# Kernel optimization log

Hardware: AMD Instinct MI355X
Metric: run time of the kernel (lower is better)

Reference implementation:

```python
import jax, jax.numpy as jnp
import numpy as np

B, T, C = 4, 2048, 768
H, D = 12, 64          # num heads, head size
MLP = 3072
EPS = 1e-6
SCALE = C ** (-0.5)    # NOTE: source scales by n_embd**-0.5, not head_size**-0.5


def setup_inputs() -> dict:
    key = jax.random.key(0)
    ks = jax.random.split(key, 12)
    s = 0.02
    return {
        "x":     jax.random.normal(ks[0], (B, T, C), jnp.float32),
        "Wq":    jax.random.normal(ks[1], (H, C, D), jnp.float32) * s,
        "Wk":    jax.random.normal(ks[2], (H, C, D), jnp.float32) * s,
        "Wv":    jax.random.normal(ks[3], (H, C, D), jnp.float32) * s,
        "Wo":    jax.random.normal(ks[4], (H * D, C), jnp.float32) * s,
        "bo":    jnp.zeros((C,), jnp.float32),
        "ln1_g": jnp.ones((C,), jnp.float32),
        "ln1_b": jnp.zeros((C,), jnp.float32),
        "ln2_g": jnp.ones((C,), jnp.float32),
        "ln2_b": jnp.zeros((C,), jnp.float32),
        "W1":    jax.random.normal(ks[5], (C, MLP), jnp.float32) * s,
        "b1":    jnp.zeros((MLP,), jnp.float32),
        "W2":    jax.random.normal(ks[6], (MLP, C), jnp.float32) * s,
        "b2":    jnp.zeros((C,), jnp.float32),
    }


def _ln(x, g, b):
    mu = jnp.mean(x, axis=-1, keepdims=True)
    var = jnp.var(x, axis=-1, keepdims=True)
    return (x - mu) * jax.lax.rsqrt(var + EPS) * g + b


def reference(x, Wq, Wk, Wv, Wo, bo, ln1_g, ln1_b, ln2_g, ln2_b, W1, b1, W2, b2):
    xn = _ln(x, ln1_g, ln1_b)
    # batched per-head projections: [B,T,C] x [H,C,D] -> [B,H,T,D]
    q = jnp.einsum("btc,hcd->bhtd", xn, Wq)
    k = jnp.einsum("btc,hcd->bhtd", xn, Wk)
    v = jnp.einsum("btc,hcd->bhtd", xn, Wv)
    wei = jnp.einsum("bhtd,bhsd->bhts", q, k) * SCALE  # [B,H,T,T]
    wei = jax.nn.softmax(wei, axis=-1)
    attn = jnp.einsum("bhts,bhsd->bhtd", wei, v)
    # concat heads along feature dim (head order preserved)
    attn = attn.transpose(0, 2, 1, 3).reshape(B, T, H * D)
    sa = attn @ Wo + bo
    x2 = sa + x                      # residual 1 (dropout = identity in eval)
    y = _ln(x2, ln2_g, ln2_b)
    y = jax.nn.gelu(y @ W1 + b1, approximate=False) @ W2 + b2
    return x2 + y                    # residual 2
```

## Files before the change

### kernel.cpp

```cpp
#include <hip/hip_runtime.h>
#include <hip/hip_bf16.h>
#include <cstdint>
#include <cmath>

#define B_ 4
#define T_ 2048
#define C_ 768
#define H_ 12
#define D_ 64
#define MLP_ 3072
#define BT_ (B_*T_)

typedef __hip_bfloat16 hbf;
typedef __bf16 bf16_t;
typedef bf16_t bf16x8 __attribute__((ext_vector_type(8)));
typedef bf16_t bf16x4 __attribute__((ext_vector_type(4)));
typedef float f32x4 __attribute__((ext_vector_type(4)));

static __device__ __forceinline__ void load_lds16(const void* g, void* l) {
    __builtin_amdgcn_global_load_lds(
        (const __attribute__((address_space(1))) unsigned int*)g,
        (__attribute__((address_space(3))) unsigned int*)l, 16, 0, 0);
}

__global__ __launch_bounds__(256) void transpose_pack(
    const float* __restrict__ src, hbf* __restrict__ dst, int R, int S)
{
    __shared__ float tl[64 * 65];
    src += (size_t)blockIdx.z * R * S;
    dst += (size_t)blockIdx.z * R * S;
    const int r0 = blockIdx.y * 64, s0 = blockIdx.x * 64;
    const int c = threadIdx.x & 63, q = threadIdx.x >> 6;
#pragma unroll
    for (int j = 0; j < 16; ++j) {
        int r = q + j * 4;
        tl[r * 65 + c] = src[(size_t)(r0 + r) * S + s0 + c];
    }
    __syncthreads();
#pragma unroll
    for (int j = 0; j < 16; ++j) {
        int s = q + j * 4;
        dst[(size_t)(s0 + s) * R + r0 + c] = __float2bfloat16(tl[c * 65 + s]);
    }
}

__global__ __launch_bounds__(256) void ln_kernel(
    const float* __restrict__ x, const float* __restrict__ g,
    const float* __restrict__ bb, hbf* __restrict__ out)
{
    __shared__ float red[8];
    const int row = blockIdx.x;
    const float* xr = x + (size_t)row * C_;
    const int t = threadIdx.x;
    float v0 = xr[t], v1 = xr[t + 256], v2 = xr[t + 512];
    float s = v0 + v1 + v2;
    float s2 = v0 * v0 + v1 * v1 + v2 * v2;
#pragma unroll
    for (int m = 1; m < 64; m <<= 1) {
        s  += __shfl_xor(s,  m, 64);
        s2 += __shfl_xor(s2, m, 64);
    }
    if ((t & 63) == 0) { red[t >> 6] = s; red[4 + (t >> 6)] = s2; }
    __syncthreads();
    float S  = red[0] + red[1] + red[2] + red[3];
    float S2 = red[4] + red[5] + red[6] + red[7];
    float mu  = S * (1.0f / C_);
    float var = S2 * (1.0f / C_) - mu * mu;
    float inv = rsqrtf(var + 1e-6f);
    hbf* orow = out + (size_t)row * C_;
    orow[t]       = __float2bfloat16((v0 - mu) * inv * g[t]       + bb[t]);
    orow[t + 256] = __float2bfloat16((v1 - mu) * inv * g[t + 256] + bb[t + 256]);
    orow[t + 512] = __float2bfloat16((v2 - mu) * inv * g[t + 512] + bb[t + 512]);
}

template<int EPI>
__global__ __launch_bounds__(256, 2) void gemm_kernel(
    const hbf* __restrict__ A, const hbf* __restrict__ Bt,
    float* __restrict__ outF, hbf* __restrict__ outH,
    const float* __restrict__ bias, const float* __restrict__ resid,
    int M, int N, int K,
    hbf* __restrict__ qb, hbf* __restrict__ kb,
    float scale, int gx)
{
    __shared__ hbf sA0[128 * 64], sA1[128 * 64];
    __shared__ hbf sB0[128 * 64], sB1[128 * 64];
    const int tid = threadIdx.x;
    const int lane = tid & 63;
    const int wid = tid >> 6;
    const int wm = wid >> 1, wn = wid & 1;
    const int lr = lane & 15, hg = lane >> 4;
    const int bid = blockIdx.x, nwg = gridDim.x;
    const int wg = (bid & 7) * (nwg >> 3) + (bid >> 3);
    const int bx = wg % gx, by = wg / gx;
    const int row0 = by * 128;
    const int col0 = bx * 128;

    f32x4 acc[4][4] = {};

    int offG[4];
    const int Kb = K * 2;
#pragma unroll
    for (int i = 0; i < 4; ++i) {
        int c = tid + i * 256;
        offG[i] = (c >> 3) * Kb + (((c & 7) ^ ((c >> 3) & 7)) << 4);
    }
    const char* gA = (const char*)(A + (size_t)row0 * K);
    const char* gB = (const char*)(Bt + (size_t)col0 * K);

    auto stage = [&](int kt, hbf* sAd, hbf* sBd) {
        const int kb2 = kt * 128;
#pragma unroll
        for (int i = 0; i < 4; ++i) {
            load_lds16(gA + (size_t)(offG[i] + kb2), (char*)sAd + i * 4096 + wid * 1024);
            load_lds16(gB + (size_t)(offG[i] + kb2), (char*)sBd + i * 4096 + wid * 1024);
        }
    };
    auto compute = [&](const hbf* sAc, const hbf* sBc) {
#pragma unroll
        for (int kf = 0; kf < 2; ++kf) {
            const int sl = ((kf * 4 + hg) ^ (lr & 7)) << 4;
            bf16x8 af[4], bfr[4];
#pragma unroll
            for (int m = 0; m < 4; ++m)
                af[m] = *(const bf16x8*)((const char*)sAc + (wm * 64 + m * 16 + lr) * 128 + sl);
#pragma unroll
            for (int n = 0; n < 4; ++n)
                bfr[n] = *(const bf16x8*)((const char*)sBc + (wn * 64 + n * 16 + lr) * 128 + sl);
#pragma unroll
            for (int m = 0; m < 4; ++m)
#pragma unroll
                for (int n = 0; n < 4; ++n)
                    acc[m][n] = __builtin_amdgcn_mfma_f32_16x16x32_bf16(af[m], bfr[n], acc[m][n], 0, 0, 0);
        }
    };

    const int NK = K >> 6;
    stage(0, sA0, sB0);
    __syncthreads();
    for (int kt = 0; kt < NK; kt += 2) {
        stage(kt + 1, sA1, sB1);
        compute(sA0, sB0);
        __syncthreads();
        if (kt + 2 < NK) stage(kt + 2, sA0, sB0);
        compute(sA1, sB1);
        __syncthreads();
    }

#pragma unroll
    for (int m = 0; m < 4; ++m) {
#pragma unroll
        for (int n = 0; n < 4; ++n) {
#pragma unroll
            for (int j = 0; j < 4; ++j) {
                int row = row0 + wm * 64 + m * 16 + hg * 4 + j;
                int col = col0 + wn * 64 + n * 16 + lr;
                float v = acc[m][n][j];
                if constexpr (EPI == 0) {
                    outH[(size_t)row * N + col] = __float2bfloat16(v);
                } else if constexpr (EPI == 1) {
                    outF[(size_t)row * N + col] = v + bias[col] + resid[(size_t)row * N + col];
                } else if constexpr (EPI == 2) {
                    float tt = v + bias[col];
                    float ge = 0.5f * tt * (1.0f + erff(tt * 0.70710678118654752f));
                    outH[(size_t)row * N + col] = __float2bfloat16(ge);
                } else {
                    int typ = col / C_;
                    int rr = col - typ * C_;
                    int h = rr >> 6, d = rr & 63;
                    int b = row >> 11, t = row & (T_ - 1);
                    size_t bh = (size_t)b * H_ + h;
                    if (typ == 0) qb[(bh * T_ + t) * D_ + d] = __float2bfloat16(v * scale);
                    else          kb[(bh * T_ + t) * D_ + d] = __float2bfloat16(v);
                }
            }
        }
    }
}

__global__ __launch_bounds__(256, 3) void attn_kernel(
    const hbf* __restrict__ qg, const hbf* __restrict__ kg,
    const hbf* __restrict__ vg, hbf* __restrict__ outA)
{
    __shared__ hbf sK0[64 * 64], sK1[64 * 64];
    __shared__ hbf sV0[64 * 64], sV1[64 * 64];
    __shared__ hbf sP[4 * 32 * 64];
    const int tid = threadIdx.x, lane = tid & 63, wid = tid >> 6;
    const int lr = lane & 15, hg = lane >> 4;
    const int wg = (blockIdx.x & 7) * 96 + (blockIdx.x >> 3);
    const int bh = wg >> 4;
    const int b = bh / H_, h = bh - b * H_;
    const int wr0 = (wg & 15) * 128 + wid * 32;
    const hbf* qbh = qg + (size_t)bh * T_ * D_;
    const hbf* kbh = kg + (size_t)bh * T_ * D_;
    const hbf* vbh = vg + (size_t)h * 64 * BT_ + (size_t)b * T_;

    bf16x8 a_q[2][2];
#pragma unroll
    for (int m = 0; m < 2; ++m)
#pragma unroll
        for (int kf = 0; kf < 2; ++kf)
            a_q[m][kf] = *(const bf16x8*)(qbh + (size_t)(wr0 + m * 16 + lr) * D_ + kf * 32 + hg * 8);

    f32x4 o[2][4] = {};
    float mreg[2] = {-3e38f, -3e38f};
    float lrun[2] = {0.0f, 0.0f};

    int offK[2], offV[2];
#pragma unroll
    for (int i = 0; i < 2; ++i) {
        int c = tid + i * 256;
        int sw = ((c & 7) ^ ((c >> 3) & 7)) << 4;
        offK[i] = (c >> 3) * 128 + sw;
        offV[i] = (c >> 3) * (BT_ * 2) + sw;
    }
    hbf* sPw = sP + wid * (32 * 64);
    const int sl0 = ((0 * 4 + hg) ^ (lr & 7)) << 4;
    const int sl1 = ((1 * 4 + hg) ^ (lr & 7)) << 4;
    const int bcast = hg * 20;

    auto stage = [&](int itn, hbf* sKd, hbf* sVd) {
        const char* kp = (const char*)kbh + (size_t)itn * 8192;
        const char* vp = (const char*)vbh + (size_t)itn * 128;
#pragma unroll
        for (int i = 0; i < 2; ++i) {
            load_lds16(kp + offK[i], (char*)sKd + i * 4096 + wid * 1024);
            load_lds16(vp + offV[i], (char*)sVd + i * 4096 + wid * 1024);
        }
    };

    auto tile = [&](const hbf* sKc, const hbf* sVc) {
        f32x4 st[4][2] = {};
        __builtin_amdgcn_s_setprio(1);
#pragma unroll
        for (int kf = 0; kf < 2; ++kf) {
            const int sl = kf ? sl1 : sl0;
#pragma unroll
            for (int n = 0; n < 4; ++n) {
                bf16x8 ak = *(const bf16x8*)((const char*)sKc + (n * 16 + lr) * 128 + sl);
                st[n][0] = __builtin_amdgcn_mfma_f32_16x16x32_bf16(ak, a_q[0][kf], st[n][0], 0, 0, 0);
                st[n][1] = __builtin_amdgcn_mfma_f32_16x16x32_bf16(ak, a_q[1][kf], st[n][1], 0, 0, 0);
            }
        }
        __builtin_amdgcn_s_setprio(0);

#pragma unroll
        for (int m = 0; m < 2; ++m) {
            float t = st[0][m][0];
#pragma unroll
            for (int n = 0; n < 4; ++n)
#pragma unroll
                for (int j = 0; j < 4; ++j)
                    if (n + j > 0) t = fmaxf(t, st[n][m][j]);
            t = fmaxf(t, __shfl_xor(t, 16, 64));
            t = fmaxf(t, __shfl_xor(t, 32, 64));
            if (__any(t - mreg[m] > 8.0f)) {
                float nm = fmaxf(mreg[m], t);
                float fac = __expf(mreg[m] - nm);
                mreg[m] = nm;
                lrun[m] *= fac;
                float fb[4];
#pragma unroll
                for (int j = 0; j < 4; ++j)
                    fb[j] = __shfl(fac, bcast + j, 64);
#pragma unroll
                for (int nd = 0; nd < 4; ++nd)
#pragma unroll
                    for (int j = 0; j < 4; ++j)
                        o[m][nd][j] *= fb[j];
            }
            float ps = 0.0f;
            const int r = m * 16 + lr;
#pragma unroll
            for (int n = 0; n < 4; ++n) {
                float p0 = __expf(st[n][m][0] - mreg[m]);
                float p1 = __expf(st[n][m][1] - mreg[m]);
                float p2 = __expf(st[n][m][2] - mreg[m]);
                float p3 = __expf(st[n][m][3] - mreg[m]);
                ps += (p0 + p1) + (p2 + p3);
                bf16x4 w;
                w[0] = (bf16_t)p0; w[1] = (bf16_t)p1; w[2] = (bf16_t)p2; w[3] = (bf16_t)p3;
                *(bf16x4*)((char*)sPw + r * 128 +
                           (((n * 2 + (hg >> 1)) ^ (r & 7)) << 4) + ((hg & 1) * 8)) = w;
            }
            ps += __shfl_xor(ps, 16, 64);
            ps += __shfl_xor(ps, 32, 64);
            lrun[m] += ps;
        }

        __builtin_amdgcn_s_setprio(1);
#pragma unroll
        for (int kf = 0; kf < 2; ++kf) {
            const int sl = kf ? sl1 : sl0;
            bf16x8 ap0 = *(const bf16x8*)((const char*)sPw + lr * 128 + sl);
            bf16x8 ap1 = *(const bf16x8*)((const char*)sPw + (16 + lr) * 128 + sl);
#pragma unroll
            for (int nd = 0; nd < 4; ++nd) {
                bf16x8 bv = *(const bf16x8*)((const char*)sVc + (nd * 16 + lr) * 128 + sl);
                o[0][nd] = __builtin_amdgcn_mfma_f32_16x16x32_bf16(ap0, bv, o[0][nd], 0, 0, 0);
                o[1][nd] = __builtin_amdgcn_mfma_f32_16x16x32_bf16(ap1, bv, o[1][nd], 0, 0, 0);
            }
        }
        __builtin_amdgcn_s_setprio(0);
    };

    const int NT = T_ / 64;
    stage(0, sK0, sV0);
    __syncthreads();
    for (int it = 0; it < NT; it += 2) {
        stage(it + 1, sK1, sV1);
        tile(sK0, sV0);
        __syncthreads();
        if (it + 2 < NT) stage(it + 2, sK0, sV0);
        tile(sK1, sV1);
        __syncthreads();
    }

    float lb[2][4];
#pragma unroll
    for (int m = 0; m < 2; ++m)
#pragma unroll
        for (int j = 0; j < 4; ++j)
            lb[m][j] = __shfl(lrun[m], bcast + j, 64);
#pragma unroll
    for (int m = 0; m < 2; ++m)
#pragma unroll
        for (int nd = 0; nd < 4; ++nd)
#pragma unroll
            for (int j = 0; j < 4; ++j) {
                int row = wr0 + m * 16 + hg * 4 + j;
                int col = nd * 16 + lr;
                float val = o[m][nd][j] / lb[m][j];
                outA[((size_t)(b * T_ + row)) * C_ + h * D_ + col] = __float2bfloat16(val);
            }
}

extern "C" void kernel_launch(void* const* d_in, const int* in_sizes, int n_in,
                              void* d_out, int out_size, void* d_ws, size_t ws_size,
                              hipStream_t stream)
{
    const float* x    = (const float*)d_in[0];
    const float* Wq   = (const float*)d_in[1];
    const float* Wk   = (const float*)d_in[2];
    const float* Wv   = (const float*)d_in[3];
    const float* Wo   = (const float*)d_in[4];
    const float* bo   = (const float*)d_in[5];
    const float* ln1g = (const float*)d_in[6];
    const float* ln1b = (const float*)d_in[7];
    const float* ln2g = (const float*)d_in[8];
    const float* ln2b = (const float*)d_in[9];
    const float* W1   = (const float*)d_in[10];
    const float* b1   = (const float*)d_in[11];
    const float* W2   = (const float*)d_in[12];
    const float* b2   = (const float*)d_in[13];
    float* out = (float*)d_out;
    char* ws = (char*)d_ws;

    hbf*  xn    = (hbf*)(ws + 0);
    hbf*  WqkT  = (hbf*)(ws + 12582912);
    hbf*  WvT   = (hbf*)(ws + 14942208);
    hbf*  qb    = (hbf*)(ws + 16121856);
    hbf*  kb    = (hbf*)(ws + 28704768);
    hbf*  vT    = (hbf*)(ws + 41287680);
    hbf*  h1    = (hbf*)(ws + 0);
    hbf*  attnB = (hbf*)(ws + 53870592);
    hbf*  yln   = (hbf*)(ws + 53870592);
    float* x2   = (float*)(ws + 66453504);
    hbf*  WoT   = (hbf*)(ws + 91619328);
    hbf*  W1T   = (hbf*)(ws + 92798976);
    hbf*  W2T   = (hbf*)(ws + 97517568);

    const float SCALE = 0.036084391824351615f;

    transpose_pack<<<dim3(1, 12, 12), 256, 0, stream>>>(Wq, WqkT, 768, 64);
    transpose_pack<<<dim3(1, 12, 12), 256, 0, stream>>>(Wk, WqkT + 768 * 768, 768, 64);
    transpose_pack<<<dim3(1, 12, 12), 256, 0, stream>>>(Wv, WvT, 768, 64);
    transpose_pack<<<dim3(12, 12, 1), 256, 0, stream>>>(Wo, WoT, 768, 768);
    transpose_pack<<<dim3(48, 12, 1), 256, 0, stream>>>(W1, W1T, 768, 3072);
    transpose_pack<<<dim3(12, 48, 1), 256, 0, stream>>>(W2, W2T, 3072, 768);
    ln_kernel<<<8192, 256, 0, stream>>>(x, ln1g, ln1b, xn);
    gemm_kernel<3><<<768, 256, 0, stream>>>(xn, WqkT, nullptr, nullptr, nullptr, nullptr,
        8192, 1536, 768, qb, kb, SCALE, 12);
    gemm_kernel<0><<<384, 256, 0, stream>>>(WvT, xn, nullptr, vT, nullptr, nullptr,
        768, BT_, 768, nullptr, nullptr, 1.0f, 64);
    attn_kernel<<<768, 256, 0, stream>>>(qb, kb, vT, attnB);
    gemm_kernel<1><<<384, 256, 0, stream>>>(attnB, WoT, x2, nullptr, bo, x,
        8192, 768, 768, nullptr, nullptr, 1.0f, 6);
    ln_kernel<<<8192, 256, 0, stream>>>(x2, ln2g, ln2b, yln);
    gemm_kernel<2><<<1536, 256, 0, stream>>>(yln, W1T, nullptr, h1, b1, nullptr,
        8192, 3072, 768, nullptr, nullptr, 1.0f, 24);
    gemm_kernel<1><<<384, 256, 0, stream>>>(h1, W2T, out, nullptr, b2, x2,
        8192, 768, 3072, nullptr, nullptr, 1.0f, 6);
}
```

Baseline: 303.2 us.

## Single-buffer GEMM LDS, halve attention rows per wave, merge QKV packing

The GEMM moves from double-buffered to single-buffered LDS and raises its occupancy hint from 2 to 3 blocks per CU, giving up load/compute overlap for more resident waves. The attention kernel now gives each wave 16 query rows instead of 32, doubling the grid to 1536 blocks, shrinking the P buffer and raising the occupancy hint to 4. K/V tiles are therefore reused across fewer query rows, so K/V traffic per query doubles. The three Q/K/V weight transpose launches are merged into one kernel to cut launch overhead.

```diff
diff --git a/kernel.cpp b/kernel.cpp
--- a/kernel.cpp
+++ b/kernel.cpp
@@ -41,6 +41,31 @@
     for (int j = 0; j < 16; ++j) {
         int s = q + j * 4;
         dst[(size_t)(s0 + s) * R + r0 + c] = __float2bfloat16(tl[c * 65 + s]);
+    }
+}
+
+__global__ __launch_bounds__(256) void pack_qkv3(
+    const float* __restrict__ Wq, const float* __restrict__ Wk,
+    const float* __restrict__ Wv, hbf* __restrict__ WqkT, hbf* __restrict__ WvT)
+{
+    __shared__ float tl[64 * 65];
+    const int z = blockIdx.z;
+    const int mtx = z / 12, head = z - mtx * 12;
+    const float* src = (mtx == 0 ? Wq : mtx == 1 ? Wk : Wv) + (size_t)head * 49152;
+    hbf* dst = (mtx == 2) ? (WvT + (size_t)head * 49152)
+                          : (WqkT + (size_t)(mtx * 12 + head) * 49152);
+    const int r0 = blockIdx.y * 64;
+    const int c = threadIdx.x & 63, q = threadIdx.x >> 6;
+#pragma unroll
+    for (int j = 0; j < 16; ++j) {
+        int r = q + j * 4;
+        tl[r * 65 + c] = src[(size_t)(r0 + r) * 64 + c];
+    }
+    __syncthreads();
+#pragma unroll
+    for (int j = 0; j < 16; ++j) {
+        int s = q + j * 4;
+        dst[(size_t)s * 768 + r0 + c] = __float2bfloat16(tl[c * 65 + s]);
     }
 }
 
@@ -74,7 +99,7 @@
 }
 
 template<int EPI>
-__global__ __launch_bounds__(256, 2) void gemm_kernel(
+__global__ __launch_bounds__(256, 3) void gemm_kernel(
     const hbf* __restrict__ A, const hbf* __restrict__ Bt,
     float* __restrict__ outF, hbf* __restrict__ outH,
     const float* __restrict__ bias, const float* __restrict__ resid,
@@ -82,8 +107,8 @@
     hbf* __restrict__ qb, hbf* __restrict__ kb,
     float scale, int gx)
 {
-    __shared__ hbf sA0[128 * 64], sA1[128 * 64];
-    __shared__ hbf sB0[128 * 64], sB1[128 * 64];
+    __shared__ hbf sA[128 * 64];
+    __shared__ hbf sB[128 * 64];
     const int tid = threadIdx.x;
     const int lane = tid & 63;
     const int wid = tid >> 6;
@@ -107,43 +132,37 @@
     const char* gA = (const char*)(A + (size_t)row0 * K);
     const char* gB = (const char*)(Bt + (size_t)col0 * K);
 
-    auto stage = [&](int kt, hbf* sAd, hbf* sBd) {
+    auto stage = [&](int kt) {
         const int kb2 = kt * 128;
 #pragma unroll
         for (int i = 0; i < 4; ++i) {
-            load_lds16(gA + (size_t)(offG[i] + kb2), (char*)sAd + i * 4096 + wid * 1024);
-            load_lds16(gB + (size_t)(offG[i] + kb2), (char*)sBd + i * 4096 + wid * 1024);
+            load_lds16(gA + (size_t)(offG[i] + kb2), (char*)sA + i * 4096 + wid * 1024);
+            load_lds16(gB + (size_t)(offG[i] + kb2), (char*)sB + i * 4096 + wid * 1024);
         }
     };
-    auto compute = [&](const hbf* sAc, const hbf* sBc) {
+
+    const int NK = K >> 6;
+    stage(0);
+    for (int kt = 0; kt < NK; ++kt) {
+        __syncthreads();
 #pragma unroll
         for (int kf = 0; kf < 2; ++kf) {
             const int sl = ((kf * 4 + hg) ^ (lr & 7)) << 4;
             bf16x8 af[4], bfr[4];
 #pragma unroll
             for (int m = 0; m < 4; ++m)
-                af[m] = *(const bf16x8*)((const char*)sAc + (wm * 64 + m * 16 + lr) * 128 + sl);
+                af[m] = *(const bf16x8*)((const char*)sA + (wm * 64 + m * 16 + lr) * 128 + sl);
 #pragma unroll
             for (int n = 0; n < 4; ++n)
-                bfr[n] = *(const bf16x8*)((const char*)sBc + (wn * 64 + n * 16 + lr) * 128 + sl);
+                bfr[n] = *(const bf16x8*)((const char*)sB + (wn * 64 + n * 16 + lr) * 128 + sl);
 #pragma unroll
             for (int m = 0; m < 4; ++m)
 #pragma unroll
                 for (int n = 0; n < 4; ++n)
                     acc[m][n] = __builtin_amdgcn_mfma_f32_16x16x32_bf16(af[m], bfr[n], acc[m][n], 0, 0, 0);
         }
-    };
-
-    const int NK = K >> 6;
-    stage(0, sA0, sB0);
-    __syncthreads();
-    for (int kt = 0; kt < NK; kt += 2) {
-        stage(kt + 1, sA1, sB1);
-        compute(sA0, sB0);
         __syncthreads();
-        if (kt + 2 < NK) stage(kt + 2, sA0, sB0);
-        compute(sA1, sB1);
-        __syncthreads();
+        if (kt + 1 < NK) stage(kt + 1);
     }
 
 #pragma unroll
@@ -177,33 +196,31 @@
     }
 }
 
-__global__ __launch_bounds__(256, 3) void attn_kernel(
+__global__ __launch_bounds__(256, 4) void attn_kernel(
     const hbf* __restrict__ qg, const hbf* __restrict__ kg,
     const hbf* __restrict__ vg, hbf* __restrict__ outA)
 {
     __shared__ hbf sK0[64 * 64], sK1[64 * 64];
     __shared__ hbf sV0[64 * 64], sV1[64 * 64];
-    __shared__ hbf sP[4 * 32 * 64];
+    __shared__ hbf sP[4 * 16 * 64];
     const int tid = threadIdx.x, lane = tid & 63, wid = tid >> 6;
     const int lr = lane & 15, hg = lane >> 4;
-    const int wg = (blockIdx.x & 7) * 96 + (blockIdx.x >> 3);
-    const int bh = wg >> 4;
+    const int wg = (blockIdx.x & 7) * 192 + (blockIdx.x >> 3);
+    const int bh = wg >> 5;
     const int b = bh / H_, h = bh - b * H_;
-    const int wr0 = (wg & 15) * 128 + wid * 32;
+    const int wr0 = (wg & 31) * 64 + wid * 16;
     const hbf* qbh = qg + (size_t)bh * T_ * D_;
     const hbf* kbh = kg + (size_t)bh * T_ * D_;
     const hbf* vbh = vg + (size_t)h * 64 * BT_ + (size_t)b * T_;
 
-    bf16x8 a_q[2][2];
-#pragma unroll
-    for (int m = 0; m < 2; ++m)
-#pragma unroll
-        for (int kf = 0; kf < 2; ++kf)
-            a_q[m][kf] = *(const bf16x8*)(qbh + (size_t)(wr0 + m * 16 + lr) * D_ + kf * 32 + hg * 8);
-
-    f32x4 o[2][4] = {};
-    float mreg[2] = {-3e38f, -3e38f};
-    float lrun[2] = {0.0f, 0.0f};
+    bf16x8 a_q[2];
+#pragma unroll
+    for (int kf = 0; kf < 2; ++kf)
+        a_q[kf] = *(const bf16x8*)(qbh + (size_t)(wr0 + lr) * D_ + kf * 32 + hg * 8);
+
+    f32x4 o[4] = {};
+    float mreg = -3e38f;
+    float lrun = 0.0f;
 
     int offK[2], offV[2];
 #pragma unroll
@@ -213,7 +230,7 @@
         offK[i] = (c >> 3) * 128 + sw;
         offV[i] = (c >> 3) * (BT_ * 2) + sw;
     }
-    hbf* sPw = sP + wid * (32 * 64);
+    hbf* sPw = sP + wid * (16 * 64);
     const int sl0 = ((0 * 4 + hg) ^ (lr & 7)) << 4;
     const int sl1 = ((1 * 4 + hg) ^ (lr & 7)) << 4;
     const int bcast = hg * 20;
@@ -229,7 +246,7 @@
     };
 
     auto tile = [&](const hbf* sKc, const hbf* sVc) {
-        f32x4 st[4][2] = {};
+        f32x4 st[4] = {};
         __builtin_amdgcn_s_setprio(1);
 #pragma unroll
         for (int kf = 0; kf < 2; ++kf) {
@@ -237,67 +254,60 @@
 #pragma unroll
             for (int n = 0; n < 4; ++n) {
                 bf16x8 ak = *(const bf16x8*)((const char*)sKc + (n * 16 + lr) * 128 + sl);
-                st[n][0] = __builtin_amdgcn_mfma_f32_16x16x32_bf16(ak, a_q[0][kf], st[n][0], 0, 0, 0);
-                st[n][1] = __builtin_amdgcn_mfma_f32_16x16x32_bf16(ak, a_q[1][kf], st[n][1], 0, 0, 0);
+                st[n] = __builtin_amdgcn_mfma_f32_16x16x32_bf16(ak, a_q[kf], st[n], 0, 0, 0);
             }
         }
         __builtin_amdgcn_s_setprio(0);
 
-#pragma unroll
-        for (int m = 0; m < 2; ++m) {
-            float t = st[0][m][0];
-#pragma unroll
-            for (int n = 0; n < 4; ++n)
+        float t = st[0][0];
+#pragma unroll
+        for (int n = 0; n < 4; ++n)
+#pragma unroll
+            for (int j = 0; j < 4; ++j)
+                if (n + j > 0) t = fmaxf(t, st[n][j]);
+        t = fmaxf(t, __shfl_xor(t, 16, 64));
+        t = fmaxf(t, __shfl_xor(t, 32, 64));
+        if (__any(t - mreg > 8.0f)) {
+            float nm = fmaxf(mreg, t);
+            float fac = __expf(mreg - nm);
+            mreg = nm;
+            lrun *= fac;
+            float fb[4];
+#pragma unroll
+            for (int j = 0; j < 4; ++j)
+                fb[j] = __shfl(fac, bcast + j, 64);
+#pragma unroll
+            for (int nd = 0; nd < 4; ++nd)
 #pragma unroll
                 for (int j = 0; j < 4; ++j)
-                    if (n + j > 0) t = fmaxf(t, st[n][m][j]);
-            t = fmaxf(t, __shfl_xor(t, 16, 64));
-            t = fmaxf(t, __shfl_xor(t, 32, 64));
-            if (__any(t - mreg[m] > 8.0f)) {
-                float nm = fmaxf(mreg[m], t);
-                float fac = __expf(mreg[m] - nm);
-                mreg[m] = nm;
-                lrun[m] *= fac;
-                float fb[4];
-#pragma unroll
-                for (int j = 0; j < 4; ++j)
-                    fb[j] = __shfl(fac, bcast + j, 64);
-#pragma unroll
-                for (int nd = 0; nd < 4; ++nd)
-#pragma unroll
-                    for (int j = 0; j < 4; ++j)
-                        o[m][nd][j] *= fb[j];
-            }
-            float ps = 0.0f;
-            const int r = m * 16 + lr;
-#pragma unroll
-            for (int n = 0; n < 4; ++n) {
-                float p0 = __expf(st[n][m][0] - mreg[m]);
-                float p1 = __expf(st[n][m][1] - mreg[m]);
-                float p2 = __expf(st[n][m][2] - mreg[m]);
-                float p3 = __expf(st[n][m][3] - mreg[m]);
-                ps += (p0 + p1) + (p2 + p3);
-                bf16x4 w;
-                w[0] = (bf16_t)p0; w[1] = (bf16_t)p1; w[2] = (bf16_t)p2; w[3] = (bf16_t)p3;
-                *(bf16x4*)((char*)sPw + r * 128 +
-                           (((n * 2 + (hg >> 1)) ^ (r & 7)) << 4) + ((hg & 1) * 8)) = w;
-            }
-            ps += __shfl_xor(ps, 16, 64);
-            ps += __shfl_xor(ps, 32, 64);
-            lrun[m] += ps;
-        }
+                    o[nd][j] *= fb[j];
+        }
+        float ps = 0.0f;
+#pragma unroll
+        for (int n = 0; n < 4; ++n) {
+            float p0 = __expf(st[n][0] - mreg);
+            float p1 = __expf(st[n][1] - mreg);
+            float p2 = __expf(st[n][2] - mreg);
+            float p3 = __expf(st[n][3] - mreg);
+            ps += (p0 + p1) + (p2 + p3);
+            bf16x4 w;
+            w[0] = (bf16_t)p0; w[1] = (bf16_t)p1; w[2] = (bf16_t)p2; w[3] = (bf16_t)p3;
+            *(bf16x4*)((char*)sPw + lr * 128 +
+                       (((n * 2 + (hg >> 1)) ^ (lr & 7)) << 4) + ((hg & 1) * 8)) = w;
+        }
+        ps += __shfl_xor(ps, 16, 64);
+        ps += __shfl_xor(ps, 32, 64);
+        lrun += ps;
 
         __builtin_amdgcn_s_setprio(1);
 #pragma unroll
         for (int kf = 0; kf < 2; ++kf) {
             const int sl = kf ? sl1 : sl0;
-            bf16x8 ap0 = *(const bf16x8*)((const char*)sPw + lr * 128 + sl);
-            bf16x8 ap1 = *(const bf16x8*)((const char*)sPw + (16 + lr) * 128 + sl);
+            bf16x8 ap = *(const bf16x8*)((const char*)sPw + lr * 128 + sl);
 #pragma unroll
             for (int nd = 0; nd < 4; ++nd) {
                 bf16x8 bv = *(const bf16x8*)((const char*)sVc + (nd * 16 + lr) * 128 + sl);
-                o[0][nd] = __builtin_amdgcn_mfma_f32_16x16x32_bf16(ap0, bv, o[0][nd], 0, 0, 0);
-                o[1][nd] = __builtin_amdgcn_mfma_f32_16x16x32_bf16(ap1, bv, o[1][nd], 0, 0, 0);
+                o[nd] = __builtin_amdgcn_mfma_f32_16x16x32_bf16(ap, bv, o[nd], 0, 0, 0);
             }
         }
         __builtin_amdgcn_s_setprio(0);
@@ -315,23 +325,19 @@
         __syncthreads();
     }
 
-    float lb[2][4];
-#pragma unroll
-    for (int m = 0; m < 2; ++m)
-#pragma unroll
-        for (int j = 0; j < 4; ++j)
-            lb[m][j] = __shfl(lrun[m], bcast + j, 64);
-#pragma unroll
-    for (int m = 0; m < 2; ++m)
-#pragma unroll
-        for (int nd = 0; nd < 4; ++nd)
-#pragma unroll
-            for (int j = 0; j < 4; ++j) {
-                int row = wr0 + m * 16 + hg * 4 + j;
-                int col = nd * 16 + lr;
-                float val = o[m][nd][j] / lb[m][j];
-                outA[((size_t)(b * T_ + row)) * C_ + h * D_ + col] = __float2bfloat16(val);
-            }
+    float lb[4];
+#pragma unroll
+    for (int j = 0; j < 4; ++j)
+        lb[j] = __shfl(lrun, bcast + j, 64);
+#pragma unroll
+    for (int nd = 0; nd < 4; ++nd)
+#pragma unroll
+        for (int j = 0; j < 4; ++j) {
+            int row = wr0 + hg * 4 + j;
+            int col = nd * 16 + lr;
+            float val = o[nd][j] / lb[j];
+            outA[((size_t)(b * T_ + row)) * C_ + h * D_ + col] = __float2bfloat16(val);
+        }
 }
 
 extern "C" void kernel_launch(void* const* d_in, const int* in_sizes, int n_in,
@@ -371,9 +377,7 @@
 
     const float SCALE = 0.036084391824351615f;
 
-    transpose_pack<<<dim3(1, 12, 12), 256, 0, stream>>>(Wq, WqkT, 768, 64);
-    transpose_pack<<<dim3(1, 12, 12), 256, 0, stream>>>(Wk, WqkT + 768 * 768, 768, 64);
-    transpose_pack<<<dim3(1, 12, 12), 256, 0, stream>>>(Wv, WvT, 768, 64);
+    pack_qkv3<<<dim3(1, 12, 36), 256, 0, stream>>>(Wq, Wk, Wv, WqkT, WvT);
     transpose_pack<<<dim3(12, 12, 1), 256, 0, stream>>>(Wo, WoT, 768, 768);
     transpose_pack<<<dim3(48, 12, 1), 256, 0, stream>>>(W1, W1T, 768, 3072);
     transpose_pack<<<dim3(12, 48, 1), 256, 0, stream>>>(W2, W2T, 3072, 768);
@@ -382,7 +386,7 @@
         8192, 1536, 768, qb, kb, SCALE, 12);
     gemm_kernel<0><<<384, 256, 0, stream>>>(WvT, xn, nullptr, vT, nullptr, nullptr,
         768, BT_, 768, nullptr, nullptr, 1.0f, 64);
-    attn_kernel<<<768, 256, 0, stream>>>(qb, kb, vT, attnB);
+    attn_kernel<<<1536, 256, 0, stream>>>(qb, kb, vT, attnB);
     gemm_kernel<1><<<384, 256, 0, stream>>>(attnB, WoT, x2, nullptr, bo, x,
         8192, 768, 768, nullptr, nullptr, 1.0f, 6);
     ln_kernel<<<8192, 256, 0, stream>>>(x2, ln2g, ln2b, yln);
```

New measurement: 312.1 us. +2.9%, slower.
